# Optimization experiments

Hardware: AMD Instinct MI355X
Metric: run time of the kernel (lower is better)

## Reference

```python
import jax, jax.numpy as jnp
import numpy as np

EPS = 1e-12  # tf.nn.l2_normalize epsilon used inside keras CosineSimilarity


def _cos(a, b):
    # keras CosineSimilarity returns -cos; callers negate explicitly.
    an = a / jnp.sqrt(jnp.maximum(jnp.sum(a * a, axis=-1, keepdims=True), EPS))
    bn = b / jnp.sqrt(jnp.maximum(jnp.sum(b * b, axis=-1, keepdims=True), EPS))
    return jnp.sum(an * bn, axis=-1)


def setup_inputs() -> dict:
    key = jax.random.key(0)
    B, S, D, H, N = 1024, 200, 128, 128, 64
    ks = jax.random.split(key, 8)
    X_series = jax.random.normal(ks[0], (B, S, D), jnp.float32)
    pos_series = jax.random.normal(ks[1], (S, D), jnp.float32)
    X_item = jax.random.normal(ks[2], (B, D), jnp.float32)
    origin = jax.random.normal(ks[3], (B, N, D), jnp.float32)  # X_negative
    # contiguous-prefix validity mask (module assumes valid positions form a prefix)
    lengths = jax.random.randint(ks[4], (B,), 1, S + 1)
    valid_mask = jnp.arange(S)[None, :] < lengths[:, None]
    # learned params (GlorotUniform-scale init)
    Wp = jax.random.normal(ks[5], (D, H), jnp.float32) * 0.08
    We = jax.random.normal(ks[6], (D, H), jnp.float32) * 0.08
    z = jax.random.normal(ks[7], (H,), jnp.float32) * 0.1
    return {"X_series": X_series, "pos_series": pos_series, "X_item": X_item,
            "valid_mask": valid_mask, "origin": origin, "Wp": Wp, "We": We, "z": z}


def reference(X_series, pos_series, X_item, valid_mask, origin, Wp, We, z):
    B, S, D = X_series.shape
    # additive tanh attention: z . tanh(X_series @ We + pos_series @ Wp)
    hidden = jnp.tanh(jnp.einsum('bsd,dh->bsh', X_series, We) + (pos_series @ Wp)[None])
    scores = jnp.einsum('bsh,h->bs', hidden, z)
    scores = jnp.where(valid_mask, scores, -jnp.inf)
    attn = jax.nn.softmax(scores, axis=-1)                      # [B,S]
    attentioned = attn[:, :, None] * X_series                    # [B,S,D]
    attention_output = jnp.sum(attentioned, axis=1)              # [B,D]
    inner = jnp.sum(attention_output * X_item, axis=-1, keepdims=True)
    concated = jnp.concatenate([attention_output, inner], axis=1)  # [B,D+1]

    # ---- auxiliary loss ----
    last_idx = jnp.sum(valid_mask.astype(jnp.int32), axis=1) - 1
    last_vec = attentioned[jnp.arange(B), last_idx]              # gather_nd
    new_mask = (jnp.arange(S)[None, :] < last_idx[:, None]).astype(X_series.dtype)
    out_vec = jnp.sum(attentioned * new_mask[:, :, None], axis=1)  # [B,D]
    # keras CosineSimilarity = -cos_sim; then mapped to (x+1)/2 and used as logits
    pos_logits = (-_cos(last_vec, out_vec) + 1.0) / 2.0          # [B]
    neg_logits = (-_cos(origin, out_vec[:, None, :]) + 1.0) / 2.0  # [B,N]
    pos_loss = jax.nn.softplus(-pos_logits)  # sigmoid_xent labels=1
    neg_loss = jax.nn.softplus(neg_logits)   # sigmoid_xent labels=0
    # NB: TF reduces pos_loss over its only axis -> scalar, broadcast-added to [B]
    auxiliary_loss = jnp.sum(pos_loss) + jnp.sum(neg_loss, axis=-1)  # [B]
    return concated, auxiliary_loss
```

## Files before the change

kernel.cpp:

```cpp
#include <hip/hip_runtime.h>
#include <hip/hip_bf16.h>
#include <math.h>

#define B_ 1024
#define S_ 200
#define D_ 128
#define H_ 128
#define N_ 64

typedef __attribute__((ext_vector_type(8))) short short8;
typedef __attribute__((ext_vector_type(8))) __bf16 bf16x8;
typedef __attribute__((ext_vector_type(4))) float floatx4;

static __device__ __forceinline__ float bf2f(unsigned short u) {
    union { unsigned int i; float f; } v; v.i = ((unsigned int)u) << 16; return v.f;
}
static __device__ __forceinline__ unsigned short f2bf(float f) {
    union { float f; unsigned int u; } v; v.f = f;
    unsigned int u = v.u;
    return (unsigned short)((u + 0x7FFFu + ((u >> 16) & 1u)) >> 16);
}
static __device__ __forceinline__ float ld1(const void* p, int isbf, size_t i) {
    return isbf ? bf2f(((const unsigned short*)p)[i]) : ((const float*)p)[i];
}
static __device__ __forceinline__ float fast_tanh(float x) {
    float t = __expf(2.0f * x);
    return 1.0f - 2.0f * __builtin_amdgcn_rcpf(t + 1.0f);
}

__global__ __launch_bounds__(64) void detect_kernel(
    const void* a0, const void* a1, const void* a2, const void* a3,
    const void* a4, const void* a5, const void* a6, const void* a7,
    int* flags)
{
    int bid = blockIdx.x, t = threadIdx.x;
    if (bid == 3) {
        const unsigned char* mb = (const unsigned char*)a3;
        int f = 0;
        for (int i = t; i < 4096; i += 64)
            if ((i & 3) && mb[i]) f = 1;
        for (int off = 32; off; off >>= 1) f |= __shfl_xor(f, off, 64);
        if (t == 0) flags[3] = f;
        return;
    }
    const void* ptrs[8] = {a0, a1, a2, a3, a4, a5, a6, a7};
    const int counts[8] = {B_*S_*D_, S_*D_, B_*D_, 0, B_*N_*D_, D_*H_, D_*H_, H_};
    const unsigned int* w = (const unsigned int*)ptrs[bid];
    int words = counts[bid] / 2; if (words > 1024) words = 1024;
    int pass = 0, tot = 0;
    for (int i = t; i < words; i += 64) {
        unsigned int e = (w[i] >> 7) & 0xFF;
        tot++;
        if (e == 0 || (e >= 96 && e <= 140)) pass++;
    }
    for (int off = 32; off; off >>= 1) {
        pass += __shfl_xor(pass, off, 64);
        tot  += __shfl_xor(tot,  off, 64);
    }
    if (t == 0) flags[bid] = (pass * 4 >= tot * 3) ? 1 : 0;
}

__global__ __launch_bounds__(128) void prep_kernel(
    const void* __restrict__ We, const void* __restrict__ pos,
    const void* __restrict__ Wp, const int* __restrict__ flags,
    unsigned short* __restrict__ WeTf, float* __restrict__ pb)
{
    int blk = blockIdx.x, t = threadIdx.x;
    __shared__ unsigned short T[128][136];
    __shared__ float prow[D_];
    if (blk == 0) {
        int fWe = flags[6];
        for (int c = t; c < 2048; c += 128) {
            int d = c >> 4, h8 = (c & 15) * 8;
            short8 v;
            if (fWe) {
                v = *(const short8*)((const unsigned short*)We + d * H_ + h8);
            } else {
                const float* p = (const float*)We + d * H_ + h8;
                float4 a = ((const float4*)p)[0], b = ((const float4*)p)[1];
                v[0] = (short)f2bf(a.x); v[1] = (short)f2bf(a.y);
                v[2] = (short)f2bf(a.z); v[3] = (short)f2bf(a.w);
                v[4] = (short)f2bf(b.x); v[5] = (short)f2bf(b.y);
                v[6] = (short)f2bf(b.z); v[7] = (short)f2bf(b.w);
            }
            *(short8*)(&T[d][h8]) = v;
        }
        __syncthreads();
        for (int i = t; i < 2048; i += 128) {
            int frag = i >> 6, ln = i & 63;
            int nt = frag >> 2, kks = frag & 3;
            int h = nt * 16 + (ln & 15);
            int dbase = kks * 32 + (ln >> 4) * 8;
            short8 v;
#pragma unroll
            for (int j = 0; j < 8; ++j) v[j] = (short)T[dbase + j][h];
            *(short8*)(WeTf + (size_t)i * 8) = v;
        }
    } else {
        int s = blk - 1, h = t;
        prow[h] = ld1(pos, flags[1], (size_t)s * D_ + h);
        __syncthreads();
        float acc = 0.f;
        if (flags[5]) {
            const unsigned short* W = (const unsigned short*)Wp;
            for (int d = 0; d < D_; ++d) acc = fmaf(prow[d], bf2f(W[d * H_ + h]), acc);
        } else {
            const float* W = (const float*)Wp;
            for (int d = 0; d < D_; ++d) acc = fmaf(prow[d], W[d * H_ + h], acc);
        }
        pb[s * H_ + h] = acc;
    }
}

__global__ __launch_bounds__(256) void scores_kernel(
    const void* __restrict__ Xs, const unsigned short* __restrict__ WeTf,
    const void* __restrict__ zv, const float* __restrict__ pb,
    const int* __restrict__ flags, float* __restrict__ scores)
{
    __shared__ unsigned short Bsh[16384];
    int t = threadIdx.x;
    int lane = t & 63, w = t >> 6;
    int quad = lane >> 4, mrow = lane & 15;
    int fXs = flags[0], fz = flags[7];
    int row0 = blockIdx.x * 128 + w * 32;

    for (int i = t; i < 2048; i += 256)
        *(short8*)(Bsh + i * 8) = *(const short8*)(WeTf + (size_t)i * 8);

    float zl[8];
#pragma unroll
    for (int nt = 0; nt < 8; ++nt) zl[nt] = ld1(zv, fz, nt * 16 + mrow);

    floatx4 acc[2][8];
#pragma unroll
    for (int mt = 0; mt < 2; ++mt)
#pragma unroll
        for (int nt = 0; nt < 8; ++nt) {
            acc[mt][nt][0] = 0.f; acc[mt][nt][1] = 0.f;
            acc[mt][nt][2] = 0.f; acc[mt][nt][3] = 0.f;
        }
    __syncthreads();

#pragma unroll
    for (int kks = 0; kks < 4; ++kks) {
        bf16x8 af[2];
#pragma unroll
        for (int mt = 0; mt < 2; ++mt) {
            size_t roff = (size_t)(row0 + mt * 16 + mrow) * D_ + kks * 32 + quad * 8;
            if (fXs) {
                short8 v = *(const short8*)((const unsigned short*)Xs + roff);
                af[mt] = __builtin_bit_cast(bf16x8, v);
            } else {
                const float* p = (const float*)Xs + roff;
                float4 a = ((const float4*)p)[0], b = ((const float4*)p)[1];
                short8 v;
                v[0] = (short)f2bf(a.x); v[1] = (short)f2bf(a.y);
                v[2] = (short)f2bf(a.z); v[3] = (short)f2bf(a.w);
                v[4] = (short)f2bf(b.x); v[5] = (short)f2bf(b.y);
                v[6] = (short)f2bf(b.z); v[7] = (short)f2bf(b.w);
                af[mt] = __builtin_bit_cast(bf16x8, v);
            }
        }
#pragma unroll
        for (int nt = 0; nt < 8; ++nt) {
            short8 bv = *(const short8*)(Bsh + (((nt << 2) + kks) * 64 + lane) * 8);
            bf16x8 bf = __builtin_bit_cast(bf16x8, bv);
            acc[0][nt] = __builtin_amdgcn_mfma_f32_16x16x32_bf16(af[0], bf, acc[0][nt], 0, 0, 0);
            acc[1][nt] = __builtin_amdgcn_mfma_f32_16x16x32_bf16(af[1], bf, acc[1][nt], 0, 0, 0);
        }
    }

#pragma unroll
    for (int mt = 0; mt < 2; ++mt) {
#pragma unroll
        for (int reg = 0; reg < 4; ++reg) {
            int grow = row0 + mt * 16 + quad * 4 + reg;
            int s = grow % S_;
            const float* pbrow = pb + (size_t)s * H_;
            float rs = 0.f;
#pragma unroll
            for (int nt = 0; nt < 8; ++nt)
                rs = fmaf(fast_tanh(acc[mt][nt][reg] + pbrow[nt * 16 + mrow]), zl[nt], rs);
#pragma unroll
            for (int off = 1; off < 16; off <<= 1)
                rs += __shfl_xor(rs, off, 64);
            if (mrow == 0) scores[grow] = rs;
        }
    }
}

__global__ __launch_bounds__(256) void attnout_kernel(
    const void* __restrict__ Xs, const void* __restrict__ Xitem,
    const void* __restrict__ maskv, const void* __restrict__ origin,
    const float* __restrict__ scores, const int* __restrict__ flags,
    float* __restrict__ pos_loss, float* __restrict__ neg_sum,
    float* __restrict__ out)
{
    int b = blockIdx.x, t = threadIdx.x;
    int wv = t >> 6, lane = t & 63;
    int fXs = flags[0], fXi = flags[2], fMk = flags[3], fOr = flags[4];
    __shared__ float attn[256];
    __shared__ float att_out[D_];
    __shared__ float lastv[D_];
    __shared__ float outv[D_];
    __shared__ float partial[8][D_];
    __shared__ float p_oo[4][64];
    __shared__ float p_ov[4][64];
    __shared__ float red[16];
    __shared__ int redi[4];
    __shared__ float sc1s, sc2s, vvs;

    int nn = t >> 2, part = t & 3;
    float o_f[32];
    if (fOr) {
        const unsigned short* p = (const unsigned short*)origin + ((size_t)b * N_ + nn) * D_ + part * 32;
#pragma unroll
        for (int j = 0; j < 4; ++j) {
            uint4 u = *(const uint4*)(p + j * 8);
            o_f[j*8+0] = bf2f((unsigned short)(u.x & 0xffff));
            o_f[j*8+1] = bf2f((unsigned short)(u.x >> 16));
            o_f[j*8+2] = bf2f((unsigned short)(u.y & 0xffff));
            o_f[j*8+3] = bf2f((unsigned short)(u.y >> 16));
            o_f[j*8+4] = bf2f((unsigned short)(u.z & 0xffff));
            o_f[j*8+5] = bf2f((unsigned short)(u.z >> 16));
            o_f[j*8+6] = bf2f((unsigned short)(u.w & 0xffff));
            o_f[j*8+7] = bf2f((unsigned short)(u.w >> 16));
        }
    } else {
        const float* p = (const float*)origin + ((size_t)b * N_ + nn) * D_ + part * 32;
#pragma unroll
        for (int j = 0; j < 8; ++j) {
            float4 v = *(const float4*)(p + j * 4);
            o_f[j*4+0] = v.x; o_f[j*4+1] = v.y; o_f[j*4+2] = v.z; o_f[j*4+3] = v.w;
        }
    }

    int nz = 0;
    if (t < S_)
        nz = fMk ? (((const unsigned char*)maskv)[(size_t)b * S_ + t] != 0)
                 : (((const int*)maskv)[(size_t)b * S_ + t] != 0);
    unsigned long long bal = __ballot(nz);
    if (lane == 0) redi[wv] = __popcll(bal);
    __syncthreads();
    int length = redi[0] + redi[1] + redi[2] + redi[3];
    int last = length - 1;

    float sc = (t < length) ? scores[(size_t)b * S_ + t] : -INFINITY;
    float m = sc;
    for (int off = 32; off; off >>= 1) m = fmaxf(m, __shfl_xor(m, off, 64));
    if (lane == 0) red[wv] = m;
    __syncthreads();
    if (t == 0) sc1s = fmaxf(fmaxf(red[0], red[1]), fmaxf(red[2], red[3]));
    __syncthreads();
    float e = (t < length) ? expf(sc - sc1s) : 0.f;
    float r = e;
    for (int off = 32; off; off >>= 1) r += __shfl_xor(r, off, 64);
    __syncthreads();
    if (lane == 0) red[wv] = r;
    __syncthreads();
    if (t == 0) sc2s = red[0] + red[1] + red[2] + red[3];
    __syncthreads();
    attn[t] = e / sc2s;
    __syncthreads();

    {
        int sp = t >> 5;
        int d4 = (t & 31) * 4;
        float a0 = 0, a1 = 0, a2 = 0, a3 = 0;
        if (fXs) {
#pragma unroll 5
            for (int s = sp; s < S_; s += 8) {
                float ww = attn[s];
                uint2 u = *(const uint2*)((const unsigned short*)Xs + ((size_t)b * S_ + s) * D_ + d4);
                a0 = fmaf(ww, bf2f((unsigned short)(u.x & 0xffff)), a0);
                a1 = fmaf(ww, bf2f((unsigned short)(u.x >> 16)), a1);
                a2 = fmaf(ww, bf2f((unsigned short)(u.y & 0xffff)), a2);
                a3 = fmaf(ww, bf2f((unsigned short)(u.y >> 16)), a3);
            }
        } else {
#pragma unroll 5
            for (int s = sp; s < S_; s += 8) {
                float ww = attn[s];
                float4 u = *(const float4*)((const float*)Xs + ((size_t)b * S_ + s) * D_ + d4);
                a0 = fmaf(ww, u.x, a0);
                a1 = fmaf(ww, u.y, a1);
                a2 = fmaf(ww, u.z, a2);
                a3 = fmaf(ww, u.w, a3);
            }
        }
        partial[sp][d4] = a0; partial[sp][d4 + 1] = a1;
        partial[sp][d4 + 2] = a2; partial[sp][d4 + 3] = a3;
    }
    __syncthreads();
    if (t < D_) {
        float v = 0.f;
#pragma unroll
        for (int p = 0; p < 8; ++p) v += partial[p][t];
        att_out[t] = v;
        float lv = attn[last] * ld1(Xs, fXs, ((size_t)b * S_ + last) * D_ + t);
        lastv[t] = lv;
        outv[t] = v - lv;
    }
    __syncthreads();

    {
        float pi = (t < D_) ? att_out[t] * ld1(Xitem, fXi, (size_t)b * D_ + t) : 0.f;
        for (int off = 32; off; off >>= 1) pi += __shfl_xor(pi, off, 64);
        if (lane == 0) red[wv] = pi;
        __syncthreads();
        if (t < D_) out[(size_t)b * (D_ + 1) + t] = att_out[t];
        if (t == 0)
            out[(size_t)b * (D_ + 1) + D_] = red[0] + red[1] + red[2] + red[3];
        __syncthreads();
    }

    {
        float l_ = (t < D_) ? lastv[t] : 0.f;
        float o_ = (t < D_) ? outv[t] : 0.f;
        float r0 = l_ * l_, r1 = l_ * o_, r2 = o_ * o_;
        for (int off = 32; off; off >>= 1) {
            r0 += __shfl_xor(r0, off, 64);
            r1 += __shfl_xor(r1, off, 64);
            r2 += __shfl_xor(r2, off, 64);
        }
        if (lane == 0) { red[wv] = r0; red[4 + wv] = r1; red[8 + wv] = r2; }
        __syncthreads();
        if (t == 0) {
            float ll = red[0] + red[1] + red[2] + red[3];
            float lo = red[4] + red[5] + red[6] + red[7];
            float oo = red[8] + red[9] + red[10] + red[11];
            float cosv = lo / (sqrtf(fmaxf(ll, 1e-12f)) * sqrtf(fmaxf(oo, 1e-12f)));
            float pl = 0.5f * (1.f - cosv);
            pos_loss[b] = log1pf(expf(-pl));
            vvs = oo;
        }
        __syncthreads();
    }

    {
        float o_oo = 0.f, o_ov = 0.f;
#pragma unroll
        for (int jj = 0; jj < 32; ++jj) {
            int j = (jj + part * 8) & 31;
            float wv_ = outv[part * 32 + j];
            o_oo = fmaf(o_f[j], o_f[j], o_oo);
            o_ov = fmaf(o_f[j], wv_, o_ov);
        }
        p_oo[part][nn] = o_oo;
        p_ov[part][nn] = o_ov;
        __syncthreads();
        if (t < 64) {
            float oo = p_oo[0][t] + p_oo[1][t] + p_oo[2][t] + p_oo[3][t];
            float ov = p_ov[0][t] + p_ov[1][t] + p_ov[2][t] + p_ov[3][t];
            float cosn = ov / (sqrtf(fmaxf(oo, 1e-12f)) * sqrtf(fmaxf(vvs, 1e-12f)));
            float nl = 0.5f * (1.f - cosn);
            float nloss = log1pf(expf(nl));
            for (int off = 32; off; off >>= 1) nloss += __shfl_xor(nloss, off, 64);
            if (t == 0) neg_sum[b] = nloss;
        }
    }
}

__global__ __launch_bounds__(1024) void final_kernel(
    const float* __restrict__ pos_loss,
    const float* __restrict__ neg_sum,
    float* __restrict__ out)
{
    __shared__ float red[16];
    int t = threadIdx.x;
    float v = pos_loss[t];
    for (int off = 32; off; off >>= 1) v += __shfl_xor(v, off, 64);
    if ((t & 63) == 0) red[t >> 6] = v;
    __syncthreads();
    if (t == 0) {
        float s = 0.f;
#pragma unroll
        for (int i = 0; i < 16; ++i) s += red[i];
        red[0] = s;
    }
    __syncthreads();
    out[(size_t)B_ * (D_ + 1) + t] = red[0] + neg_sum[t];
}

extern "C" void kernel_launch(void* const* d_in, const int* in_sizes, int n_in,
                              void* d_out, int out_size, void* d_ws, size_t ws_size,
                              hipStream_t stream) {
    const void* Xs     = d_in[0];
    const void* pos    = d_in[1];
    const void* Xitem  = d_in[2];
    const void* mask   = d_in[3];
    const void* origin = d_in[4];
    const void* Wp     = d_in[5];
    const void* We     = d_in[6];
    const void* zv     = d_in[7];

    int*   flags    = (int*)d_ws;
    unsigned short* WeTf = (unsigned short*)((char*)d_ws + 128);
    float* pb       = (float*)((char*)d_ws + 128 + 32768);
    float* scores   = pb + 25600;
    float* pos_loss = scores + 204800;
    float* neg_sum  = pos_loss + B_;
    float* out = (float*)d_out;

    detect_kernel<<<8, 64, 0, stream>>>(Xs, pos, Xitem, mask, origin, Wp, We, zv, flags);
    prep_kernel<<<201, 128, 0, stream>>>(We, pos, Wp, flags, WeTf, pb);
    scores_kernel<<<(B_ * S_) / 128, 256, 0, stream>>>(Xs, WeTf, zv, pb, flags, scores);
    attnout_kernel<<<B_, 256, 0, stream>>>(Xs, Xitem, mask, origin, scores, flags,
                                           pos_loss, neg_sum, out);
    final_kernel<<<1, 1024, 0, stream>>>(pos_loss, neg_sum, out);
}
```

Before: 268.1 us.

## Precompute sequence lengths and skip masked rows in scores and attention sum

Measured after the change: 280.9 us. 4.8% more time.

```diff
diff --git a/kernel.cpp b/kernel.cpp
--- a/kernel.cpp
+++ b/kernel.cpp
@@ -58,6 +58,28 @@
         tot  += __shfl_xor(tot,  off, 64);
     }
     if (t == 0) flags[bid] = (pass * 4 >= tot * 3) ? 1 : 0;
+}
+
+__global__ __launch_bounds__(256) void lengths_kernel(
+    const void* __restrict__ maskv, const int* __restrict__ flags,
+    int* __restrict__ lengths)
+{
+    int wv = threadIdx.x >> 6, lane = threadIdx.x & 63;
+    int fMk = flags[3];
+    int base = blockIdx.x * 64 + wv * 16;
+    for (int bb = 0; bb < 16; ++bb) {
+        int b = base + bb;
+        int nz = 0;
+        if (fMk) {
+            const unsigned char* mb = (const unsigned char*)maskv + (size_t)b * S_;
+            for (int i = lane; i < S_; i += 64) nz += (mb[i] != 0);
+        } else {
+            const int* mi = (const int*)maskv + (size_t)b * S_;
+            for (int i = lane; i < S_; i += 64) nz += (mi[i] != 0);
+        }
+        for (int off = 32; off; off >>= 1) nz += __shfl_xor(nz, off, 64);
+        if (lane == 0) lengths[b] = nz;
+    }
 }
 
 __global__ __launch_bounds__(128) void prep_kernel(
@@ -115,7 +137,8 @@
 __global__ __launch_bounds__(256) void scores_kernel(
     const void* __restrict__ Xs, const unsigned short* __restrict__ WeTf,
     const void* __restrict__ zv, const float* __restrict__ pb,
-    const int* __restrict__ flags, float* __restrict__ scores)
+    const int* __restrict__ flags, const int* __restrict__ lengths,
+    float* __restrict__ scores)
 {
     __shared__ unsigned short Bsh[16384];
     int t = threadIdx.x;
@@ -130,26 +153,27 @@
     float zl[8];
 #pragma unroll
     for (int nt = 0; nt < 8; ++nt) zl[nt] = ld1(zv, fz, nt * 16 + mrow);
-
-    floatx4 acc[2][8];
-#pragma unroll
-    for (int mt = 0; mt < 2; ++mt)
+    __syncthreads();
+
+#pragma unroll
+    for (int mt = 0; mt < 2; ++mt) {
+        int r = row0 + mt * 16 + mrow;
+        int bidx = r / S_, s_ = r - bidx * S_;
+        bool valid = s_ < lengths[bidx];
+        if (!__any(valid)) continue;
+
+        floatx4 acc[8];
 #pragma unroll
         for (int nt = 0; nt < 8; ++nt) {
-            acc[mt][nt][0] = 0.f; acc[mt][nt][1] = 0.f;
-            acc[mt][nt][2] = 0.f; acc[mt][nt][3] = 0.f;
-        }
-    __syncthreads();
-
-#pragma unroll
-    for (int kks = 0; kks < 4; ++kks) {
-        bf16x8 af[2];
-#pragma unroll
-        for (int mt = 0; mt < 2; ++mt) {
-            size_t roff = (size_t)(row0 + mt * 16 + mrow) * D_ + kks * 32 + quad * 8;
+            acc[nt][0] = 0.f; acc[nt][1] = 0.f; acc[nt][2] = 0.f; acc[nt][3] = 0.f;
+        }
+#pragma unroll
+        for (int kks = 0; kks < 4; ++kks) {
+            bf16x8 af;
+            size_t roff = (size_t)r * D_ + kks * 32 + quad * 8;
             if (fXs) {
                 short8 v = *(const short8*)((const unsigned short*)Xs + roff);
-                af[mt] = __builtin_bit_cast(bf16x8, v);
+                af = __builtin_bit_cast(bf16x8, v);
             } else {
                 const float* p = (const float*)Xs + roff;
                 float4 a = ((const float4*)p)[0], b = ((const float4*)p)[1];
@@ -158,20 +182,15 @@
                 v[2] = (short)f2bf(a.z); v[3] = (short)f2bf(a.w);
                 v[4] = (short)f2bf(b.x); v[5] = (short)f2bf(b.y);
                 v[6] = (short)f2bf(b.z); v[7] = (short)f2bf(b.w);
-                af[mt] = __builtin_bit_cast(bf16x8, v);
+                af = __builtin_bit_cast(bf16x8, v);
             }
-        }
-#pragma unroll
-        for (int nt = 0; nt < 8; ++nt) {
-            short8 bv = *(const short8*)(Bsh + (((nt << 2) + kks) * 64 + lane) * 8);
-            bf16x8 bf = __builtin_bit_cast(bf16x8, bv);
-            acc[0][nt] = __builtin_amdgcn_mfma_f32_16x16x32_bf16(af[0], bf, acc[0][nt], 0, 0, 0);
-            acc[1][nt] = __builtin_amdgcn_mfma_f32_16x16x32_bf16(af[1], bf, acc[1][nt], 0, 0, 0);
-        }
-    }
-
-#pragma unroll
-    for (int mt = 0; mt < 2; ++mt) {
+#pragma unroll
+            for (int nt = 0; nt < 8; ++nt) {
+                short8 bv = *(const short8*)(Bsh + (((nt << 2) + kks) * 64 + lane) * 8);
+                bf16x8 bf = __builtin_bit_cast(bf16x8, bv);
+                acc[nt] = __builtin_amdgcn_mfma_f32_16x16x32_bf16(af, bf, acc[nt], 0, 0, 0);
+            }
+        }
 #pragma unroll
         for (int reg = 0; reg < 4; ++reg) {
             int grow = row0 + mt * 16 + quad * 4 + reg;
@@ -180,7 +199,7 @@
             float rs = 0.f;
 #pragma unroll
             for (int nt = 0; nt < 8; ++nt)
-                rs = fmaf(fast_tanh(acc[mt][nt][reg] + pbrow[nt * 16 + mrow]), zl[nt], rs);
+                rs = fmaf(fast_tanh(acc[nt][reg] + pbrow[nt * 16 + mrow]), zl[nt], rs);
 #pragma unroll
             for (int off = 1; off < 16; off <<= 1)
                 rs += __shfl_xor(rs, off, 64);
@@ -191,14 +210,14 @@
 
 __global__ __launch_bounds__(256) void attnout_kernel(
     const void* __restrict__ Xs, const void* __restrict__ Xitem,
-    const void* __restrict__ maskv, const void* __restrict__ origin,
-    const float* __restrict__ scores, const int* __restrict__ flags,
+    const void* __restrict__ origin, const float* __restrict__ scores,
+    const int* __restrict__ flags, const int* __restrict__ lengths,
     float* __restrict__ pos_loss, float* __restrict__ neg_sum,
     float* __restrict__ out)
 {
     int b = blockIdx.x, t = threadIdx.x;
     int wv = t >> 6, lane = t & 63;
-    int fXs = flags[0], fXi = flags[2], fMk = flags[3], fOr = flags[4];
+    int fXs = flags[0], fXi = flags[2], fOr = flags[4];
     __shared__ float attn[256];
     __shared__ float att_out[D_];
     __shared__ float lastv[D_];
@@ -207,7 +226,6 @@
     __shared__ float p_oo[4][64];
     __shared__ float p_ov[4][64];
     __shared__ float red[16];
-    __shared__ int redi[4];
     __shared__ float sc1s, sc2s, vvs;
 
     int nn = t >> 2, part = t & 3;
@@ -235,14 +253,7 @@
         }
     }
 
-    int nz = 0;
-    if (t < S_)
-        nz = fMk ? (((const unsigned char*)maskv)[(size_t)b * S_ + t] != 0)
-                 : (((const int*)maskv)[(size_t)b * S_ + t] != 0);
-    unsigned long long bal = __ballot(nz);
-    if (lane == 0) redi[wv] = __popcll(bal);
-    __syncthreads();
-    int length = redi[0] + redi[1] + redi[2] + redi[3];
+    int length = lengths[b];
     int last = length - 1;
 
     float sc = (t < length) ? scores[(size_t)b * S_ + t] : -INFINITY;
@@ -269,7 +280,7 @@
         float a0 = 0, a1 = 0, a2 = 0, a3 = 0;
         if (fXs) {
 #pragma unroll 5
-            for (int s = sp; s < S_; s += 8) {
+            for (int s = sp; s < length; s += 8) {
                 float ww = attn[s];
                 uint2 u = *(const uint2*)((const unsigned short*)Xs + ((size_t)b * S_ + s) * D_ + d4);
                 a0 = fmaf(ww, bf2f((unsigned short)(u.x & 0xffff)), a0);
@@ -279,7 +290,7 @@
             }
         } else {
 #pragma unroll 5
-            for (int s = sp; s < S_; s += 8) {
+            for (int s = sp; s < length; s += 8) {
                 float ww = attn[s];
                 float4 u = *(const float4*)((const float*)Xs + ((size_t)b * S_ + s) * D_ + d4);
                 a0 = fmaf(ww, u.x, a0);
@@ -400,12 +411,14 @@
     float* scores   = pb + 25600;
     float* pos_loss = scores + 204800;
     float* neg_sum  = pos_loss + B_;
+    int*   lengths  = (int*)(neg_sum + B_);
     float* out = (float*)d_out;
 
     detect_kernel<<<8, 64, 0, stream>>>(Xs, pos, Xitem, mask, origin, Wp, We, zv, flags);
+    lengths_kernel<<<16, 256, 0, stream>>>(mask, flags, lengths);
     prep_kernel<<<201, 128, 0, stream>>>(We, pos, Wp, flags, WeTf, pb);
-    scores_kernel<<<(B_ * S_) / 128, 256, 0, stream>>>(Xs, WeTf, zv, pb, flags, scores);
-    attnout_kernel<<<B_, 256, 0, stream>>>(Xs, Xitem, mask, origin, scores, flags,
+    scores_kernel<<<(B_ * S_) / 128, 256, 0, stream>>>(Xs, WeTf, zv, pb, flags, lengths, scores);
+    attnout_kernel<<<B_, 256, 0, stream>>>(Xs, Xitem, origin, scores, flags, lengths,
                                            pos_loss, neg_sum, out);
     final_kernel<<<1, 1024, 0, stream>>>(pos_loss, neg_sum, out);
 }
```
